# Kernel tuning notes

Hardware: AMD Instinct MI355X
Metric: run time of the kernel (lower is better)

## Reference

```python
import jax, jax.numpy as jnp
import numpy as np
from jax import lax

B, T, E, H, V = 1024, 128, 300, 100, 50000
K = 4  # topk in catch()
NEG_INF = -1e30


def setup_inputs() -> dict:
    key = jax.random.key(0)
    ks = jax.random.split(key, 12)
    word_id = jax.random.randint(ks[0], (B, T), 0, V, dtype=jnp.int32)
    sen_len = jax.random.randint(ks[1], (B,), K, T + 1, dtype=jnp.int32)  # >= K for topk
    label_word_id = jax.random.randint(ks[2], (B, 1), 0, V, dtype=jnp.int32)
    emb = jax.random.normal(ks[3], (V, E), jnp.float32) * 0.1
    W_ih = jax.random.normal(ks[4], (4 * H, E), jnp.float32) * 0.05
    W_hh = jax.random.normal(ks[5], (4 * H, H), jnp.float32) * 0.05
    b_ih = jax.random.normal(ks[6], (4 * H,), jnp.float32) * 0.05
    b_hh = jax.random.normal(ks[7], (4 * H,), jnp.float32) * 0.05
    lin_W = jax.random.normal(ks[8], (6, H), jnp.float32) * 0.1
    lin_b = jax.random.normal(ks[9], (6,), jnp.float32) * 0.1
    ll_W = jax.random.normal(ks[10], (H, E), jnp.float32) * 0.05
    ll_b = jax.random.normal(ks[11], (H,), jnp.float32) * 0.05
    return dict(word_id=word_id, sen_len=sen_len, label_word_id=label_word_id,
                emb=emb, W_ih=W_ih, W_hh=W_hh, b_ih=b_ih, b_hh=b_hh,
                lin_W=lin_W, lin_b=lin_b, ll_W=ll_W, ll_b=ll_b)


def _lstm(x, W_ih, W_hh, b_ih, b_hh):
    # x: (B, T, E) -> out: (B, T, H). Single layer, pytorch gate order i,f,g,o.
    b = b_ih + b_hh
    def step(carry, x_t):
        h, c = carry
        gates = x_t @ W_ih.T + h @ W_hh.T + b  # (B, 4H)
        i, f, g, o = jnp.split(gates, 4, axis=-1)
        c = jax.nn.sigmoid(f) * c + jax.nn.sigmoid(i) * jnp.tanh(g)
        h = jax.nn.sigmoid(o) * jnp.tanh(c)
        return (h, c), h
    h0 = jnp.zeros((x.shape[0], W_hh.shape[1]), x.dtype)
    (_, _), hs = lax.scan(step, (h0, h0), x.transpose(1, 0, 2))
    return hs.transpose(1, 0, 2)


def reference(word_id, sen_len, label_word_id, emb, W_ih, W_hh, b_ih, b_hh,
              lin_W, lin_b, ll_W, ll_b):
    word_vec = emb[word_id]                      # (B, T, E)
    out = _lstm(word_vec, W_ih, W_hh, b_ih, b_hh)  # (B, T, H)

    # last valid hidden state -> linear
    last = out[jnp.arange(out.shape[0]), sen_len - 1]  # (B, H)
    out_f = last @ lin_W.T + lin_b               # (B, 6)

    # label vector through llinear
    label_vec = emb[label_word_id[:, 0]] @ ll_W.T + ll_b  # (B, H)

    # --- catch(), vectorized ---
    scores = jnp.einsum('bth,bh->bt', out, label_vec)     # (B, T)
    valid = jnp.arange(out.shape[1])[None, :] < sen_len[:, None]  # (B, T)
    vals, idx = lax.top_k(jnp.where(valid, scores, NEG_INF), K)   # (B, K)
    s_value = jnp.take_along_axis(out, idx[:, :, None], axis=1)   # (B, K, H)
    pos = jnp.sum(s_value * vals[:, :, None], axis=1)             # (B, H)

    # neg: valid positions excluding topk; original bug: vector_list accumulates
    # across the batch loop -> cumulative sum over batch dimension.
    top_mask = jnp.zeros(valid.shape, bool).at[
        jnp.arange(valid.shape[0])[:, None], idx].set(True)
    neg_mask = valid & ~top_mask                                   # (B, T)
    per_neg = jnp.einsum('bth,bt->bh', out, neg_mask.astype(out.dtype))
    neg = jnp.cumsum(per_neg, axis=0)                              # (B, H)

    l_rep = pos @ lin_W.T + lin_b
    r_rep = neg @ lin_W.T + lin_b
    return (out_f, l_rep, r_rep)
```

## Files before the change

kernel.cpp:

```cpp
#include <hip/hip_runtime.h>
#include <hip/hip_bf16.h>
#include <cstdint>

#define Bn   1024
#define Tn   128
#define En   300
#define Hn   100
#define Vn   50000
#define G4n  400
#define MPn  50048
#define NPn  448

typedef __bf16 bf16x8 __attribute__((ext_vector_type(8)));
typedef _Float16 half8 __attribute__((ext_vector_type(8)));
typedef _Float16 half2v __attribute__((ext_vector_type(2)));
typedef float  f32x4  __attribute__((ext_vector_type(4)));

#define OFF_TABLE  0ull
#define OFF_WFRAG  44800000ull
#define OFF_WFRAGB 44914688ull
#define OFF_LLWT   45201408ull
#define OFF_LV     45321408ull
#define OFF_PN6    45731008ull

__device__ __forceinline__ float sigf(float x) {
    return __builtin_amdgcn_rcpf(1.0f + __expf(-x));
}
__device__ __forceinline__ float tanhfast(float x) {
    return 1.0f - 2.0f * __builtin_amdgcn_rcpf(__expf(2.0f * x) + 1.0f);
}

#define BAR_LDS() do {                                         \
    asm volatile("s_waitcnt lgkmcnt(0)" ::: "memory");          \
    __builtin_amdgcn_s_barrier();                               \
    asm volatile("" ::: "memory");                              \
} while (0)

#define DPP_ADD_SHL(v, N) do {                                                     \
    int _s = __builtin_amdgcn_update_dpp(0, __builtin_bit_cast(int, (v)),          \
                                         0x100 | (N), 0xF, 0xF, true);             \
    (v) += __builtin_bit_cast(float, _s);                                          \
} while (0)

__global__ void k_prep(const float* __restrict__ W_ih, const float* __restrict__ W_hh,
                       const float* __restrict__ llW,
                       uint4* __restrict__ wfrag, uint4* __restrict__ wfragB,
                       float* __restrict__ llwt) {
    int idx = blockIdx.x * 256 + threadIdx.x;
    if (idx < 28 * 4 * 64) {
        int lane = idx & 63, tk = idx >> 6;
        int nt = tk >> 2, kc = tk & 3;
        int n = nt * 16 + (lane & 15);
        int k0 = kc * 32 + (lane >> 4) * 8;
        int q = n & 3, u = n >> 2;
        union { _Float16 h[8]; uint4 v; } pk;
#pragma unroll
        for (int j = 0; j < 8; j++) {
            int k = k0 + j;
            pk.h[j] = (_Float16)((u < Hn && k < Hn) ? W_hh[(size_t)(q * Hn + u) * Hn + k] : 0.0f);
        }
        wfrag[idx] = pk.v;
    }
    if (idx < 10 * 28 * 64) {
        int lane = idx & 63, tk = idx >> 6;
        int kc = tk / 28, nsg = tk - kc * 28;
        int n = nsg * 16 + (lane & 15);
        int k0 = kc * 32 + (lane >> 4) * 8;
        int q = n & 3, u = n >> 2;
        union { __bf16 h[8]; uint4 v; } pk;
#pragma unroll
        for (int j = 0; j < 8; j++) {
            int k = k0 + j;
            pk.h[j] = (__bf16)((u < Hn && k < En) ? W_ih[(size_t)(q * Hn + u) * En + k] : 0.0f);
        }
        wfragB[idx] = pk.v;
    }
    if (idx < En * Hn) {
        int k = idx / Hn, h = idx - k * Hn;
        llwt[idx] = llW[(size_t)h * En + k];
    }
}

__global__ __launch_bounds__(256, 2) void k_table(
    const float* __restrict__ emb, const uint4* __restrict__ wfragB,
    const float* __restrict__ b_ih, const float* __restrict__ b_hh,
    _Float16* __restrict__ table) {
    __shared__ __bf16 a_sh[64][328];
    const int tid = threadIdx.x;
    const int mt = blockIdx.x >> 1, nh = blockIdx.x & 1;

#pragma unroll
    for (int it = 0; it < 5; it++) {
        int x = it * 256 + tid;
        int row = x / 20, seg = x - row * 20;
        int gr = mt * 64 + row;
        const float* ar = emb + (size_t)(gr < Vn ? gr : Vn - 1) * En;
        int c0 = seg * 16;
        union { __bf16 h[16]; bf16x8 v[2]; } pk;
#pragma unroll
        for (int g = 0; g < 4; g++) {
            int c = c0 + g * 4;
            if (c + 4 <= En) {
                float4 f = *(const float4*)(ar + c);
                pk.h[g * 4 + 0] = (__bf16)f.x; pk.h[g * 4 + 1] = (__bf16)f.y;
                pk.h[g * 4 + 2] = (__bf16)f.z; pk.h[g * 4 + 3] = (__bf16)f.w;
            } else {
                pk.h[g * 4 + 0] = (__bf16)0.f; pk.h[g * 4 + 1] = (__bf16)0.f;
                pk.h[g * 4 + 2] = (__bf16)0.f; pk.h[g * 4 + 3] = (__bf16)0.f;
            }
        }
        *(bf16x8*)&a_sh[row][c0] = pk.v[0];
        *(bf16x8*)&a_sh[row][c0 + 8] = pk.v[1];
    }
    __syncthreads();

    const int wv = tid >> 6, l = tid & 63;
    const int c16 = l & 15, quad = l >> 4;
    f32x4 acc[14];
#pragma unroll
    for (int i = 0; i < 14; i++) acc[i] = (f32x4){0.f, 0.f, 0.f, 0.f};

    uint4 bcur[14];
#pragma unroll
    for (int ns = 0; ns < 14; ns++) bcur[ns] = wfragB[((0 * 28 + nh * 14 + ns) << 6) + l];

    for (int kc = 0; kc < 10; kc++) {
        uint4 bnxt[14];
        if (kc < 9) {
#pragma unroll
            for (int ns = 0; ns < 14; ns++) bnxt[ns] = wfragB[(((kc + 1) * 28 + nh * 14 + ns) << 6) + l];
        }
        bf16x8 af = *(const bf16x8*)&a_sh[wv * 16 + c16][kc * 32 + quad * 8];
#pragma unroll
        for (int ns = 0; ns < 14; ns++)
            acc[ns] = __builtin_amdgcn_mfma_f32_16x16x32_bf16(af, __builtin_bit_cast(bf16x8, bcur[ns]), acc[ns], 0, 0, 0);
        if (kc < 9) {
#pragma unroll
            for (int ns = 0; ns < 14; ns++) bcur[ns] = bnxt[ns];
        }
    }
#pragma unroll
    for (int ns = 0; ns < 14; ns++) {
        int n = (nh * 14 + ns) * 16 + c16;
        int q = n & 3, u = n >> 2;
        if (u < Hn) {
            int j = q * Hn + u;
            float bias = b_ih[j] + b_hh[j];
#pragma unroll
            for (int r = 0; r < 4; r++) {
                int m = mt * 64 + wv * 16 + quad * 4 + r;
                if (m < Vn) table[(size_t)m * NPn + n] = (_Float16)(acc[ns][r] + bias);
            }
        }
    }
}

__global__ void k_label(const int* __restrict__ lwid, const float* __restrict__ emb,
                        const float* __restrict__ llwt, const float* __restrict__ llb,
                        float* __restrict__ lv) {
    __shared__ float er[En];
    __shared__ float part[Hn];
    int b = blockIdx.x;
    int lid = lwid[b];
    for (int k = threadIdx.x; k < En; k += 256) er[k] = emb[(size_t)lid * En + k];
    __syncthreads();
    int h = threadIdx.x & 127, half = threadIdx.x >> 7;
    float acc = 0.f;
    if (h < Hn) {
        int k0 = half * 150, k1 = k0 + 150;
        for (int k = k0; k < k1; k++) acc += er[k] * llwt[k * Hn + h];
        if (half == 1) part[h] = acc;
    }
    __syncthreads();
    if (h < Hn && half == 0) lv[(size_t)b * Hn + h] = acc + part[h] + llb[h];
}

__global__ __launch_bounds__(512, 2) void k_lstm(
    const int* __restrict__ word_id, const int* __restrict__ sen_len,
    const _Float16* __restrict__ table, const uint4* __restrict__ wfrag,
    const float* __restrict__ lv, const float* __restrict__ linW,
    const float* __restrict__ linb, float* __restrict__ pn6,
    float* __restrict__ d_out) {
    __shared__ __align__(16) float    gbufs[8][320];
    __shared__ __align__(16) _Float16 h_cur[2][4][144];
    __shared__ __align__(16) _Float16 oh_lds[4][12832];
    __shared__ __align__(16) float    spw[4][Tn][8];
    __shared__ int      widc[4][Tn];
    __shared__ float    pos_sh[4][Hn];
    __shared__ float    lasth_sh[4][Hn];
    __shared__ float    neg_sh[4][Hn];
    __shared__ float    tk_val[4][4];
    __shared__ int      tk_idx[4][4];

    const int tid = threadIdx.x;
    const int w = tid >> 6, l = tid & 63;
    const int c16 = l & 15, quad = l >> 4;
    const int b0 = blockIdx.x * 4;

    for (int i = tid; i < 576; i += 512) ((uint32_t*)h_cur)[i] = 0u;
    { int imb = tid >> 7, it = tid & 127; widc[imb][it] = word_id[(b0 + imb) * Tn + it] * NPn; }

    const bool has4 = (w == 0);
    const int TB = has4 ? 0 : 4 + 3 * (w - 1);
    const int UB = TB * 4;
    const int ITEMS = has4 ? 16 : 12;

    half8 bfr[4][4];
#pragma unroll
    for (int kc = 0; kc < 4; kc++) {
        bfr[0][kc] = __builtin_bit_cast(half8, wfrag[((TB + 0) * 4 + kc) * 64 + l]);
        bfr[1][kc] = __builtin_bit_cast(half8, wfrag[((TB + 1) * 4 + kc) * 64 + l]);
        bfr[2][kc] = __builtin_bit_cast(half8, wfrag[((TB + 2) * 4 + kc) * 64 + l]);
        if (has4) bfr[3][kc] = __builtin_bit_cast(half8, wfrag[((TB + 3) * 4 + kc) * 64 + l]);
    }

    const int iu = l >> 2, mb = l & 3;
    const int u = UB + iu;
    const bool act = (iu < ITEMS);
    const int slen = act ? sen_len[b0 + mb] : 0;
    const float lt_reg = act ? lv[(size_t)(b0 + mb) * Hn + u] : 0.f;
    float* gb = &gbufs[w][0];
    const _Float16* tb_u = table + u * 4;

    __syncthreads();

    uint2 xq = {0, 0}, xq1 = {0, 0};
    if (act) {
        xq  = *(const uint2*)(tb_u + (size_t)widc[mb][0]);
        xq1 = *(const uint2*)(tb_u + (size_t)widc[mb][1]);
    }

    float c_reg = 0.f, sumh = 0.f, lasth = 0.f;
    float p_carry = 0.f;

    for (int t = 0; t < Tn; t++) {
        const _Float16* hp = &h_cur[t & 1][0][0];
        f32x4 acc[4];
        {
            half8 af0 = *(const half8*)(hp + (c16 & 3) * 144 + quad * 8);
            acc[0] = __builtin_amdgcn_mfma_f32_16x16x32_f16(af0, bfr[0][0], (f32x4){0.f, 0.f, 0.f, 0.f}, 0, 0, 0);
            acc[1] = __builtin_amdgcn_mfma_f32_16x16x32_f16(af0, bfr[1][0], (f32x4){0.f, 0.f, 0.f, 0.f}, 0, 0, 0);
            acc[2] = __builtin_amdgcn_mfma_f32_16x16x32_f16(af0, bfr[2][0], (f32x4){0.f, 0.f, 0.f, 0.f}, 0, 0, 0);
            if (has4) acc[3] = __builtin_amdgcn_mfma_f32_16x16x32_f16(af0, bfr[3][0], (f32x4){0.f, 0.f, 0.f, 0.f}, 0, 0, 0);
        }
#pragma unroll
        for (int kc = 1; kc < 4; kc++) {
            half8 af = *(const half8*)(hp + (c16 & 3) * 144 + kc * 32 + quad * 8);
            acc[0] = __builtin_amdgcn_mfma_f32_16x16x32_f16(af, bfr[0][kc], acc[0], 0, 0, 0);
            acc[1] = __builtin_amdgcn_mfma_f32_16x16x32_f16(af, bfr[1][kc], acc[1], 0, 0, 0);
            acc[2] = __builtin_amdgcn_mfma_f32_16x16x32_f16(af, bfr[2][kc], acc[2], 0, 0, 0);
            if (has4) acc[3] = __builtin_amdgcn_mfma_f32_16x16x32_f16(af, bfr[3][kc], acc[3], 0, 0, 0);
        }
        if (l < 16) {
            int adr0 = (c16 >> 2) * 5 + (c16 & 3);
#pragma unroll
            for (int r = 0; r < 4; r++) gb[r * 80 + adr0] = acc[0][r];
#pragma unroll
            for (int r = 0; r < 4; r++) gb[r * 80 + adr0 + 20] = acc[1][r];
#pragma unroll
            for (int r = 0; r < 4; r++) gb[r * 80 + adr0 + 40] = acc[2][r];
            if (has4) {
#pragma unroll
                for (int r = 0; r < 4; r++) gb[r * 80 + adr0 + 60] = acc[3][r];
            }
        }
        {
            float pr = p_carry;
            DPP_ADD_SHL(pr, 4);
            DPP_ADD_SHL(pr, 8);
            pr += __shfl_down(pr, 32, 64);
            pr += __shfl_down(pr, 16, 64);
            if (l < 4 && t > 0) spw[l][t - 1][w] = pr;
        }
        float p = 0.f;
        if (act) {
            int base = mb * 80 + iu * 5;
            half2v x01 = __builtin_bit_cast(half2v, xq.x);
            half2v x23 = __builtin_bit_cast(half2v, xq.y);
            float gi = gb[base] + (float)x01.x;
            float gf = gb[base + 1] + (float)x01.y;
            float gg = gb[base + 2] + (float)x23.x;
            float go = gb[base + 3] + (float)x23.y;
            float c = sigf(gf) * c_reg + sigf(gi) * tanhfast(gg);
            c_reg = c;
            float hh = sigf(go) * tanhfast(c);
            _Float16 h16 = (_Float16)hh;
            h_cur[(t + 1) & 1][mb][u] = h16;
            oh_lds[mb][t * Hn + u] = h16;
            if (t < slen) sumh += hh;
            if (t == slen - 1) lasth = hh;
            p = hh * lt_reg;
            int tn2 = (t + 2 < Tn) ? t + 2 : Tn - 1;
            xq = xq1;
            xq1 = *(const uint2*)(tb_u + (size_t)widc[mb][tn2]);
        }
        p_carry = p;
        BAR_LDS();
    }
    {
        float pr = p_carry;
        DPP_ADD_SHL(pr, 4);
        DPP_ADD_SHL(pr, 8);
        pr += __shfl_down(pr, 32, 64);
        pr += __shfl_down(pr, 16, 64);
        if (l < 4) spw[l][Tn - 1][w] = pr;
    }
    __syncthreads();
    if (w < 4) {
        int sl = sen_len[b0 + w];
        float4 a0 = *(const float4*)&spw[w][l][0];
        float4 a1 = *(const float4*)&spw[w][l][4];
        float4 c0 = *(const float4*)&spw[w][l + 64][0];
        float4 c1 = *(const float4*)&spw[w][l + 64][4];
        float sa = (a0.x + a0.y + a0.z + a0.w) + (a1.x + a1.y + a1.z + a1.w);
        float sb = (c0.x + c0.y + c0.z + c0.w) + (c1.x + c1.y + c1.z + c1.w);
        float s0 = (l < sl) ? sa : -1e30f;
        float s1 = (l + 64 < sl) ? sb : -1e30f;
        bool tk0 = false, tk1 = false;
#pragma unroll
        for (int p4 = 0; p4 < 4; p4++) {
            float v = tk0 ? -1e30f : s0;
            int ix = l;
            float v1 = tk1 ? -1e30f : s1;
            if (v1 > v) { v = v1; ix = l + 64; }
            for (int off = 32; off; off >>= 1) {
                float ov = __shfl_down(v, off, 64);
                int oi = __shfl_down(ix, off, 64);
                if (ov > v || (ov == v && oi < ix)) { v = ov; ix = oi; }
            }
            v = __shfl(v, 0, 64);
            ix = __shfl(ix, 0, 64);
            if (l == 0) { tk_val[w][p4] = v; tk_idx[w][p4] = ix; }
            if (ix == l) tk0 = true;
            if (ix == l + 64) tk1 = true;
        }
    }
    __syncthreads();
    if (act) {
        float pos = 0.f, nsum = sumh;
#pragma unroll
        for (int p4 = 0; p4 < 4; p4++) {
            int ix = tk_idx[mb][p4];
            float r = (float)oh_lds[mb][ix * Hn + u];
            pos += tk_val[mb][p4] * r;
            nsum -= r;
        }
        pos_sh[mb][u] = pos;
        lasth_sh[mb][u] = lasth;
        neg_sh[mb][u] = nsum;
    }
    __syncthreads();
    if (tid < 72) {
        int which = tid / 24, r = tid - which * 24;
        int pmb = r / 6, o = r - pmb * 6;
        const float* src = (which == 0) ? &lasth_sh[pmb][0]
                         : (which == 1) ? &pos_sh[pmb][0] : &neg_sh[pmb][0];
        float acc2 = (which == 2) ? 0.f : linb[o];
        for (int uu = 0; uu < Hn; uu++) acc2 += src[uu] * linW[o * Hn + uu];
        if (which == 0)      d_out[(b0 + pmb) * 6 + o] = acc2;
        else if (which == 1) d_out[Bn * 6 + (b0 + pmb) * 6 + o] = acc2;
        else                 pn6[(b0 + pmb) * 6 + o] = acc2;
    }
}

__global__ __launch_bounds__(1024) void k_scan6(const float* __restrict__ pn6,
                                                const float* __restrict__ linb,
                                                float* __restrict__ d_out) {
    __shared__ float wsum[16];
    __shared__ float wpre[16];
    int o = blockIdx.x, t = threadIdx.x;
    int lane = t & 63, wv = t >> 6;
    float v = pn6[t * 6 + o];
#pragma unroll
    for (int off = 1; off < 64; off <<= 1) {
        float x = __shfl_up(v, off, 64);
        if (lane >= off) v += x;
    }
    if (lane == 63) wsum[wv] = v;
    __syncthreads();
    if (t < 16) {
        float s = wsum[t];
#pragma unroll
        for (int off = 1; off < 16; off <<= 1) {
            float x = __shfl_up(s, off, 64);
            if (t >= off) s += x;
        }
        wpre[t] = s;
    }
    __syncthreads();
    float pre = wv ? wpre[wv - 1] : 0.f;
    d_out[2 * Bn * 6 + t * 6 + o] = v + pre + linb[o];
}

extern "C" void kernel_launch(void* const* d_in, const int* in_sizes, int n_in,
                              void* d_out, int out_size, void* d_ws, size_t ws_size,
                              hipStream_t stream) {
    const int*   word_id = (const int*)d_in[0];
    const int*   sen_len = (const int*)d_in[1];
    const int*   lwid    = (const int*)d_in[2];
    const float* emb     = (const float*)d_in[3];
    const float* W_ih    = (const float*)d_in[4];
    const float* W_hh    = (const float*)d_in[5];
    const float* b_ih    = (const float*)d_in[6];
    const float* b_hh    = (const float*)d_in[7];
    const float* linW    = (const float*)d_in[8];
    const float* linb    = (const float*)d_in[9];
    const float* llW     = (const float*)d_in[10];
    const float* llb     = (const float*)d_in[11];

    char* ws = (char*)d_ws;
    _Float16* table  = (_Float16*)(ws + OFF_TABLE);
    uint4*    wfrag  = (uint4*)(ws + OFF_WFRAG);
    uint4*    wfragB = (uint4*)(ws + OFF_WFRAGB);
    float*    llwt   = (float*)(ws + OFF_LLWT);
    float*    lvp    = (float*)(ws + OFF_LV);
    float*    pn6    = (float*)(ws + OFF_PN6);
    float*    outp   = (float*)d_out;

    k_prep<<<118, 256, 0, stream>>>(W_ih, W_hh, llW, wfrag, wfragB, llwt);
    k_table<<<(MPn / 64) * 2, 256, 0, stream>>>(emb, wfragB, b_ih, b_hh, table);
    k_label<<<Bn, 256, 0, stream>>>(lwid, emb, llwt, llb, lvp);
    k_lstm<<<Bn / 4, 512, 0, stream>>>(word_id, sen_len, table, wfrag, lvp, linW, linb, pn6, outp);
    k_scan6<<<6, 1024, 0, stream>>>(pn6, linb, outp);
}
```

Measured before the change: 294.0 us.

## Swap MFMA operands so gate outputs stay in registers, dropping LDS gate buffer

The recurrent matmul now puts the weight fragments in the A operand and h in the B operand, so each lane's accumulator holds all four gates (i,f,g,o) of one unit for one batch row. The per-step round-trip through the LDS gate buffer (gbufs) is removed and lanes select their accumulator by duplicate index. The lane-to-unit mapping and the score reduction (xor shuffles instead of DPP plus shfl_down) change to match. The aim is less LDS traffic and latency on the sequential critical path. In exchange, only 48 or 64 of the 64 lanes do elementwise work and extra selects are needed.

After: 269.6 us. 8.3% less time.

```diff
diff --git a/kernel.cpp b/kernel.cpp
--- a/kernel.cpp
+++ b/kernel.cpp
@@ -34,12 +34,6 @@
     asm volatile("s_waitcnt lgkmcnt(0)" ::: "memory");          \
     __builtin_amdgcn_s_barrier();                               \
     asm volatile("" ::: "memory");                              \
-} while (0)
-
-#define DPP_ADD_SHL(v, N) do {                                                     \
-    int _s = __builtin_amdgcn_update_dpp(0, __builtin_bit_cast(int, (v)),          \
-                                         0x100 | (N), 0xF, 0xF, true);             \
-    (v) += __builtin_bit_cast(float, _s);                                          \
 } while (0)
 
 __global__ void k_prep(const float* __restrict__ W_ih, const float* __restrict__ W_hh,
@@ -181,7 +175,6 @@
     const float* __restrict__ lv, const float* __restrict__ linW,
     const float* __restrict__ linb, float* __restrict__ pn6,
     float* __restrict__ d_out) {
-    __shared__ __align__(16) float    gbufs[8][320];
     __shared__ __align__(16) _Float16 h_cur[2][4][144];
     __shared__ __align__(16) _Float16 oh_lds[4][12832];
     __shared__ __align__(16) float    spw[4][Tn][8];
@@ -202,8 +195,7 @@
 
     const bool has4 = (w == 0);
     const int TB = has4 ? 0 : 4 + 3 * (w - 1);
-    const int UB = TB * 4;
-    const int ITEMS = has4 ? 16 : 12;
+    const int NT = has4 ? 4 : 3;
 
     half8 bfr[4][4];
 #pragma unroll
@@ -214,12 +206,11 @@
         if (has4) bfr[3][kc] = __builtin_bit_cast(half8, wfrag[((TB + 3) * 4 + kc) * 64 + l]);
     }
 
-    const int iu = l >> 2, mb = l & 3;
-    const int u = UB + iu;
-    const bool act = (iu < ITEMS);
+    const int mb = c16 & 3, dup = c16 >> 2;
+    const bool act = (dup < NT);
+    const int u = (TB + dup) * 4 + quad;
     const int slen = act ? sen_len[b0 + mb] : 0;
     const float lt_reg = act ? lv[(size_t)(b0 + mb) * Hn + u] : 0.f;
-    float* gb = &gbufs[w][0];
     const _Float16* tb_u = table + u * 4;
 
     __syncthreads();
@@ -235,52 +226,47 @@
 
     for (int t = 0; t < Tn; t++) {
         const _Float16* hp = &h_cur[t & 1][0][0];
-        f32x4 acc[4];
-        {
-            half8 af0 = *(const half8*)(hp + (c16 & 3) * 144 + quad * 8);
-            acc[0] = __builtin_amdgcn_mfma_f32_16x16x32_f16(af0, bfr[0][0], (f32x4){0.f, 0.f, 0.f, 0.f}, 0, 0, 0);
-            acc[1] = __builtin_amdgcn_mfma_f32_16x16x32_f16(af0, bfr[1][0], (f32x4){0.f, 0.f, 0.f, 0.f}, 0, 0, 0);
-            acc[2] = __builtin_amdgcn_mfma_f32_16x16x32_f16(af0, bfr[2][0], (f32x4){0.f, 0.f, 0.f, 0.f}, 0, 0, 0);
-            if (has4) acc[3] = __builtin_amdgcn_mfma_f32_16x16x32_f16(af0, bfr[3][0], (f32x4){0.f, 0.f, 0.f, 0.f}, 0, 0, 0);
-        }
-#pragma unroll
-        for (int kc = 1; kc < 4; kc++) {
-            half8 af = *(const half8*)(hp + (c16 & 3) * 144 + kc * 32 + quad * 8);
-            acc[0] = __builtin_amdgcn_mfma_f32_16x16x32_f16(af, bfr[0][kc], acc[0], 0, 0, 0);
-            acc[1] = __builtin_amdgcn_mfma_f32_16x16x32_f16(af, bfr[1][kc], acc[1], 0, 0, 0);
-            acc[2] = __builtin_amdgcn_mfma_f32_16x16x32_f16(af, bfr[2][kc], acc[2], 0, 0, 0);
-            if (has4) acc[3] = __builtin_amdgcn_mfma_f32_16x16x32_f16(af, bfr[3][kc], acc[3], 0, 0, 0);
-        }
-        if (l < 16) {
-            int adr0 = (c16 >> 2) * 5 + (c16 & 3);
-#pragma unroll
-            for (int r = 0; r < 4; r++) gb[r * 80 + adr0] = acc[0][r];
-#pragma unroll
-            for (int r = 0; r < 4; r++) gb[r * 80 + adr0 + 20] = acc[1][r];
-#pragma unroll
-            for (int r = 0; r < 4; r++) gb[r * 80 + adr0 + 40] = acc[2][r];
-            if (has4) {
-#pragma unroll
-                for (int r = 0; r < 4; r++) gb[r * 80 + adr0 + 60] = acc[3][r];
-            }
-        }
+        half8 hf0 = *(const half8*)(hp + (c16 & 3) * 144 + 0 * 32 + quad * 8);
+        half8 hf1 = *(const half8*)(hp + (c16 & 3) * 144 + 1 * 32 + quad * 8);
+        half8 hf2 = *(const half8*)(hp + (c16 & 3) * 144 + 2 * 32 + quad * 8);
+        half8 hf3 = *(const half8*)(hp + (c16 & 3) * 144 + 3 * 32 + quad * 8);
+        f32x4 acc0, acc1, acc2, acc3;
+        acc0 = __builtin_amdgcn_mfma_f32_16x16x32_f16(bfr[0][0], hf0, (f32x4){0.f, 0.f, 0.f, 0.f}, 0, 0, 0);
+        acc1 = __builtin_amdgcn_mfma_f32_16x16x32_f16(bfr[1][0], hf0, (f32x4){0.f, 0.f, 0.f, 0.f}, 0, 0, 0);
+        acc2 = __builtin_amdgcn_mfma_f32_16x16x32_f16(bfr[2][0], hf0, (f32x4){0.f, 0.f, 0.f, 0.f}, 0, 0, 0);
+        if (has4) acc3 = __builtin_amdgcn_mfma_f32_16x16x32_f16(bfr[3][0], hf0, (f32x4){0.f, 0.f, 0.f, 0.f}, 0, 0, 0);
+        acc0 = __builtin_amdgcn_mfma_f32_16x16x32_f16(bfr[0][1], hf1, acc0, 0, 0, 0);
+        acc1 = __builtin_amdgcn_mfma_f32_16x16x32_f16(bfr[1][1], hf1, acc1, 0, 0, 0);
+        acc2 = __builtin_amdgcn_mfma_f32_16x16x32_f16(bfr[2][1], hf1, acc2, 0, 0, 0);
+        if (has4) acc3 = __builtin_amdgcn_mfma_f32_16x16x32_f16(bfr[3][1], hf1, acc3, 0, 0, 0);
+        acc0 = __builtin_amdgcn_mfma_f32_16x16x32_f16(bfr[0][2], hf2, acc0, 0, 0, 0);
+        acc1 = __builtin_amdgcn_mfma_f32_16x16x32_f16(bfr[1][2], hf2, acc1, 0, 0, 0);
+        acc2 = __builtin_amdgcn_mfma_f32_16x16x32_f16(bfr[2][2], hf2, acc2, 0, 0, 0);
+        if (has4) acc3 = __builtin_amdgcn_mfma_f32_16x16x32_f16(bfr[3][2], hf2, acc3, 0, 0, 0);
+        acc0 = __builtin_amdgcn_mfma_f32_16x16x32_f16(bfr[0][3], hf3, acc0, 0, 0, 0);
+        acc1 = __builtin_amdgcn_mfma_f32_16x16x32_f16(bfr[1][3], hf3, acc1, 0, 0, 0);
+        acc2 = __builtin_amdgcn_mfma_f32_16x16x32_f16(bfr[2][3], hf3, acc2, 0, 0, 0);
+        if (has4) acc3 = __builtin_amdgcn_mfma_f32_16x16x32_f16(bfr[3][3], hf3, acc3, 0, 0, 0);
         {
             float pr = p_carry;
-            DPP_ADD_SHL(pr, 4);
-            DPP_ADD_SHL(pr, 8);
-            pr += __shfl_down(pr, 32, 64);
-            pr += __shfl_down(pr, 16, 64);
+            pr += __shfl_xor(pr, 4, 64);
+            pr += __shfl_xor(pr, 8, 64);
+            pr += __shfl_xor(pr, 16, 64);
+            pr += __shfl_xor(pr, 32, 64);
             if (l < 4 && t > 0) spw[l][t - 1][w] = pr;
         }
+        f32x4 g = acc0;
+        g = (dup == 1) ? acc1 : g;
+        g = (dup == 2) ? acc2 : g;
+        if (has4) g = (dup == 3) ? acc3 : g;
         float p = 0.f;
         if (act) {
-            int base = mb * 80 + iu * 5;
             half2v x01 = __builtin_bit_cast(half2v, xq.x);
             half2v x23 = __builtin_bit_cast(half2v, xq.y);
-            float gi = gb[base] + (float)x01.x;
-            float gf = gb[base + 1] + (float)x01.y;
-            float gg = gb[base + 2] + (float)x23.x;
-            float go = gb[base + 3] + (float)x23.y;
+            float gi = g[0] + (float)x01.x;
+            float gf = g[1] + (float)x01.y;
+            float gg = g[2] + (float)x23.x;
+            float go = g[3] + (float)x23.y;
             float c = sigf(gf) * c_reg + sigf(gi) * tanhfast(gg);
             c_reg = c;
             float hh = sigf(go) * tanhfast(c);
@@ -299,10 +285,10 @@
     }
     {
         float pr = p_carry;
-        DPP_ADD_SHL(pr, 4);
-        DPP_ADD_SHL(pr, 8);
-        pr += __shfl_down(pr, 32, 64);
-        pr += __shfl_down(pr, 16, 64);
+        pr += __shfl_xor(pr, 4, 64);
+        pr += __shfl_xor(pr, 8, 64);
+        pr += __shfl_xor(pr, 16, 64);
+        pr += __shfl_xor(pr, 32, 64);
         if (l < 4) spw[l][Tn - 1][w] = pr;
     }
     __syncthreads();
```
